# Optimization experiments

Measured on AMD Instinct MI355X. Metric: run time of the kernel, lower is better.

Reference implementation:

```python
import jax, jax.numpy as jnp
import numpy as np

DIGIT_RANGE = 10       # config.digitRange
SUM_RANGE = 19         # config.summationRange = 2*DIGIT_RANGE - 1
BATCH = 2_097_152


def setup_inputs() -> dict:
    key = jax.random.key(0)
    k1, k2 = jax.random.split(key)
    d1 = jax.random.normal(k1, (BATCH, DIGIT_RANGE), dtype=jnp.float32)
    d2 = jax.random.normal(k2, (BATCH, DIGIT_RANGE), dtype=jnp.float32)
    return {"d1": d1, "d2": d2}


def reference(d1, d2):
    # softmax over the digit axis (dim=0 of each per-example vector in the original)
    p1 = jax.nn.softmax(d1, axis=-1)  # [B, 10]
    p2 = jax.nn.softmax(d2, axis=-1)  # [B, 10]
    # The double loop Pd_sum[i+j] += p1[i]*p2[j] is exactly a full 1-D
    # discrete convolution producing SUM_RANGE = 2*DIGIT_RANGE-1 outputs.
    conv = jax.vmap(lambda a, b: jnp.convolve(a, b, mode="full"))
    return conv(p1, p2)  # [B, 19]
```

## Files before the change

kernel.cpp:

```cpp
#include <hip/hip_runtime.h>


constexpr int D   = 10;
constexpr int S   = 19;
constexpr int BLK = 256;

__global__ __launch_bounds__(BLK) void sumfunc_kernel(
    const float* __restrict__ d1, const float* __restrict__ d2,
    float* __restrict__ out, int n)
{
    __shared__ float so[BLK * S];

    const int tid = threadIdx.x;
    const long long row = (long long)blockIdx.x * BLK + tid;

    if (row < n) {
        const float2* p1 = reinterpret_cast<const float2*>(d1 + row * D);
        const float2* p2 = reinterpret_cast<const float2*>(d2 + row * D);
        float a[D], b[D];
        #pragma unroll
        for (int i = 0; i < 5; ++i) {
            float2 v1 = p1[i];
            float2 v2 = p2[i];
            a[2*i] = v1.x; a[2*i+1] = v1.y;
            b[2*i] = v2.x; b[2*i+1] = v2.y;
        }

        float m1 = a[0], m2 = b[0];
        #pragma unroll
        for (int i = 1; i < D; ++i) {
            m1 = fmaxf(m1, a[i]);
            m2 = fmaxf(m2, b[i]);
        }
        float s1 = 0.f, s2 = 0.f;
        #pragma unroll
        for (int i = 0; i < D; ++i) {
            a[i] = __expf(a[i] - m1); s1 += a[i];
            b[i] = __expf(b[i] - m2); s2 += b[i];
        }
        const float inv = 1.0f / (s1 * s2);

        float c[S];
        #pragma unroll
        for (int k = 0; k < S; ++k) c[k] = 0.f;
        #pragma unroll
        for (int i = 0; i < D; ++i) {
            #pragma unroll
            for (int j = 0; j < D; ++j) {
                c[i + j] = fmaf(a[i], b[j], c[i + j]);
            }
        }

        #pragma unroll
        for (int k = 0; k < S; ++k) so[tid * S + k] = c[k] * inv;
    }
    __syncthreads();

    const long long base  = (long long)blockIdx.x * (BLK * S);
    const long long total = (long long)n * S;
    #pragma unroll
    for (int k = 0; k < S; ++k) {
        long long idx = base + (long long)k * BLK + tid;
        if (idx < total) out[idx] = so[k * BLK + tid];
    }
}

extern "C" void kernel_launch(void* const* d_in, const int* in_sizes, int n_in,
                              void* d_out, int out_size, void* d_ws, size_t ws_size,
                              hipStream_t stream) {
    const float* d1 = (const float*)d_in[0];
    const float* d2 = (const float*)d_in[1];
    float* out = (float*)d_out;
    const int n = in_sizes[0] / D;
    const int grid = (n + BLK - 1) / BLK;
    sumfunc_kernel<<<grid, BLK, 0, stream>>>(d1, d2, out, n);
}
```

Before: 61.90 us.

## Stage inputs through LDS with coalesced float4 loads and vectorize output stores

After: 62.74 us. No clear change (+1.4%).

```diff
diff --git a/kernel.cpp b/kernel.cpp
--- a/kernel.cpp
+++ b/kernel.cpp
@@ -4,64 +4,97 @@
 constexpr int D   = 10;
 constexpr int S   = 19;
 constexpr int BLK = 256;
+constexpr int IN_TILE  = BLK * D;
+constexpr int OUT_TILE = BLK * S;
+constexpr int LDS_FLOATS = (2 * IN_TILE > OUT_TILE) ? 2 * IN_TILE : OUT_TILE;
 
-__global__ __launch_bounds__(BLK) void sumfunc_kernel(
+__global__ __launch_bounds__(BLK, 2) void sumfunc_kernel(
     const float* __restrict__ d1, const float* __restrict__ d2,
     float* __restrict__ out, int n)
 {
-    __shared__ float so[BLK * S];
+    __shared__ float lds[LDS_FLOATS];
 
     const int tid = threadIdx.x;
-    const long long row = (long long)blockIdx.x * BLK + tid;
+    const long long blockStart = (long long)blockIdx.x * BLK;
+    const bool full = (blockStart + BLK) <= n;
 
-    if (row < n) {
-        const float2* p1 = reinterpret_cast<const float2*>(d1 + row * D);
-        const float2* p2 = reinterpret_cast<const float2*>(d2 + row * D);
-        float a[D], b[D];
+    float a[D], b[D];
+
+    if (full) {
+        const float4* g1 = reinterpret_cast<const float4*>(d1 + blockStart * D);
+        const float4* g2 = reinterpret_cast<const float4*>(d2 + blockStart * D);
+        float4* l1 = reinterpret_cast<float4*>(lds);
+        float4* l2 = reinterpret_cast<float4*>(lds + IN_TILE);
+        l1[tid]       = g1[tid];
+        l1[tid + 256] = g1[tid + 256];
+        l2[tid]       = g2[tid];
+        l2[tid + 256] = g2[tid + 256];
+        if (tid < 128) {
+            l1[tid + 512] = g1[tid + 512];
+            l2[tid + 512] = g2[tid + 512];
+        }
+        __syncthreads();
+
+        const float2* r1 = reinterpret_cast<const float2*>(lds + tid * D);
+        const float2* r2 = reinterpret_cast<const float2*>(lds + IN_TILE + tid * D);
         #pragma unroll
         for (int i = 0; i < 5; ++i) {
-            float2 v1 = p1[i];
-            float2 v2 = p2[i];
+            float2 v1 = r1[i], v2 = r2[i];
             a[2*i] = v1.x; a[2*i+1] = v1.y;
             b[2*i] = v2.x; b[2*i+1] = v2.y;
         }
+    } else if (blockStart + tid < n) {
+        const float2* p1 = reinterpret_cast<const float2*>(d1 + (blockStart + tid) * D);
+        const float2* p2 = reinterpret_cast<const float2*>(d2 + (blockStart + tid) * D);
+        #pragma unroll
+        for (int i = 0; i < 5; ++i) {
+            float2 v1 = p1[i], v2 = p2[i];
+            a[2*i] = v1.x; a[2*i+1] = v1.y;
+            b[2*i] = v2.x; b[2*i+1] = v2.y;
+        }
+    } else {
+        #pragma unroll
+        for (int i = 0; i < D; ++i) { a[i] = 0.f; b[i] = 0.f; }
+    }
 
-        float m1 = a[0], m2 = b[0];
+    float m1 = a[0], m2 = b[0];
+    #pragma unroll
+    for (int i = 1; i < D; ++i) { m1 = fmaxf(m1, a[i]); m2 = fmaxf(m2, b[i]); }
+    float s1 = 0.f, s2 = 0.f;
+    #pragma unroll
+    for (int i = 0; i < D; ++i) {
+        a[i] = __expf(a[i] - m1); s1 += a[i];
+        b[i] = __expf(b[i] - m2); s2 += b[i];
+    }
+    const float inv = 1.0f / (s1 * s2);
+
+    float c[S];
+    #pragma unroll
+    for (int k = 0; k < S; ++k) c[k] = 0.f;
+    #pragma unroll
+    for (int i = 0; i < D; ++i) {
         #pragma unroll
-        for (int i = 1; i < D; ++i) {
-            m1 = fmaxf(m1, a[i]);
-            m2 = fmaxf(m2, b[i]);
-        }
-        float s1 = 0.f, s2 = 0.f;
-        #pragma unroll
-        for (int i = 0; i < D; ++i) {
-            a[i] = __expf(a[i] - m1); s1 += a[i];
-            b[i] = __expf(b[i] - m2); s2 += b[i];
-        }
-        const float inv = 1.0f / (s1 * s2);
+        for (int j = 0; j < D; ++j) c[i + j] = fmaf(a[i], b[j], c[i + j]);
+    }
 
-        float c[S];
-        #pragma unroll
-        for (int k = 0; k < S; ++k) c[k] = 0.f;
-        #pragma unroll
-        for (int i = 0; i < D; ++i) {
-            #pragma unroll
-            for (int j = 0; j < D; ++j) {
-                c[i + j] = fmaf(a[i], b[j], c[i + j]);
-            }
-        }
+    if (full) {
+        __syncthreads();
 
         #pragma unroll
-        for (int k = 0; k < S; ++k) so[tid * S + k] = c[k] * inv;
-    }
-    __syncthreads();
+        for (int k = 0; k < S; ++k) lds[tid * S + k] = c[k] * inv;
+        __syncthreads();
 
-    const long long base  = (long long)blockIdx.x * (BLK * S);
-    const long long total = (long long)n * S;
-    #pragma unroll
-    for (int k = 0; k < S; ++k) {
-        long long idx = base + (long long)k * BLK + tid;
-        if (idx < total) out[idx] = so[k * BLK + tid];
+        const float4* lo = reinterpret_cast<const float4*>(lds);
+        float4* go = reinterpret_cast<float4*>(out + blockStart * S);
+        go[tid]        = lo[tid];
+        go[tid + 256]  = lo[tid + 256];
+        go[tid + 512]  = lo[tid + 512];
+        go[tid + 768]  = lo[tid + 768];
+        if (tid < 192) go[tid + 1024] = lo[tid + 1024];
+    } else if (blockStart + tid < n) {
+        float* po = out + (blockStart + tid) * S;
+        #pragma unroll
+        for (int k = 0; k < S; ++k) po[k] = c[k] * inv;
     }
 }
 
```
